# Optimization experiments

Hardware: AMD Instinct MI355X
Metric: run time of the kernel (lower is better)

The kernel has to match this reference:

```python
import jax, jax.numpy as jnp
import numpy as np

D_MODEL = 1024
N_HEADS = 16
TREE_DEPTH = 5
B, T = 2, 1024


def setup_inputs() -> dict:
    key = jax.random.key(0)
    k1, k2, k3, k4 = jax.random.split(key, 4)
    sc = 1.0 / np.sqrt(D_MODEL)
    return {
        "x": jax.random.normal(k1, (B, T, D_MODEL), dtype=jnp.float32),
        "Wp": jax.random.normal(k2, (D_MODEL, N_HEADS * TREE_DEPTH), dtype=jnp.float32) * sc,
        "bp": jnp.zeros((N_HEADS * TREE_DEPTH,), dtype=jnp.float32),
        "Wv": jax.random.normal(k3, (D_MODEL, D_MODEL), dtype=jnp.float32) * sc,
        "Wo": jax.random.normal(k4, (D_MODEL, D_MODEL), dtype=jnp.float32) * sc,
    }


def reference(x, Wp, bp, Wv, Wo):
    Bc, Tc, d = x.shape
    H, Dt = N_HEADS, TREE_DEPTH
    dh = d // H
    # tree paths: (B, H, T, Dt)
    paths = jax.nn.sigmoid(x @ Wp + bp).reshape(Bc, Tc, H, Dt).transpose(0, 2, 1, 3)
    pq = paths[:, :, :, None, :]  # (B,H,T,1,Dt)
    pk = paths[:, :, None, :, :]  # (B,H,1,T,Dt)
    agree = pq * pk + (1.0 - pq) * (1.0 - pk)  # (B,H,T,T,Dt)
    sim = jnp.cumprod(agree, axis=-1).sum(axis=-1) / Dt  # (B,H,T,T)
    # causal mask (strict upper triangle -> -inf)
    causal_mask = jnp.triu(jnp.ones((Tc, Tc), dtype=bool), k=1)
    sim = jnp.where(causal_mask[None, None], -jnp.inf, sim)
    attn = jax.nn.softmax(sim, axis=-1)
    V = (x @ Wv).reshape(Bc, Tc, H, dh).transpose(0, 2, 1, 3)  # (B,H,T,dh)
    ctx = jnp.einsum("bhqk,bhkd->bhqd", attn, V)
    ctx = ctx.transpose(0, 2, 1, 3).reshape(Bc, Tc, d)
    return ctx @ Wo
```

## Files before the change

kernel.cpp:

```cpp
#include <hip/hip_runtime.h>
#include <hip/hip_bf16.h>

#define B_SZ 2
#define T_SEQ 1024
#define D_MODEL 1024
#define N_HEADS 16
#define TREE_DEPTH 5
#define DH 64

typedef __attribute__((ext_vector_type(8))) short short8;
typedef __attribute__((ext_vector_type(4))) float f32x4;

__device__ __forceinline__ ushort f2bf(float f) {
    uint32_t u = __float_as_uint(f);
    u += 0x7FFFu + ((u >> 16) & 1u);
    return (ushort)(u >> 16);
}

__device__ __forceinline__ void gll16(const void* g, void* l) {
    __builtin_amdgcn_global_load_lds(
        (const __attribute__((address_space(1))) void*)g,
        (__attribute__((address_space(3))) void*)l, 16, 0, 0);
}

__global__ __launch_bounds__(256) void prologue(
    const float* __restrict__ x, const float* __restrict__ Wv,
    const float* __restrict__ Wo, const float* __restrict__ Wp,
    ushort* __restrict__ xb, ushort* __restrict__ Wvt,
    ushort* __restrict__ Wot, ushort* __restrict__ Wpt)
{
    __shared__ __align__(16) char sm[20480];
    const int bid = blockIdx.x, tid = threadIdx.x;
    if (bid < 1024) {
        const int i = (bid * 256 + tid) * 8;
        const float4 a = *(const float4*)(x + i);
        const float4 b = *(const float4*)(x + i + 4);
        ushort o[8] = {f2bf(a.x), f2bf(a.y), f2bf(a.z), f2bf(a.w),
                       f2bf(b.x), f2bf(b.y), f2bf(b.z), f2bf(b.w)};
        *(uint4*)(xb + i) = *(const uint4*)o;
    } else if (bid < 3072) {
        const int t = bid - 1024;
        const float* W = (t < 1024) ? Wv : Wo;
        ushort* Wt = (t < 1024) ? Wvt : Wot;
        const int ti = t & 1023;
        const int n0 = (ti & 31) * 32, k0 = (ti >> 5) * 32;
        float (*tile)[33] = (float(*)[33])sm;
        const int tx = tid & 31, ty = tid >> 5;
        #pragma unroll
        for (int i = 0; i < 4; ++i)
            tile[ty + i * 8][tx] = W[(size_t)(k0 + ty + i * 8) * 1024 + n0 + tx];
        __syncthreads();
        #pragma unroll
        for (int i = 0; i < 4; ++i)
            Wt[(size_t)(n0 + ty + i * 8) * 1024 + k0 + tx] = f2bf(tile[tx][ty + i * 8]);
    } else {
        float* tile = (float*)sm;
        const int k0 = (bid - 3072) * 64;
        #pragma unroll
        for (int j = 0; j < 20; ++j) {
            const int i = tid + j * 256;
            tile[i] = Wp[(size_t)k0 * 80 + i];
        }
        __syncthreads();
        #pragma unroll
        for (int j = 0; j < 20; ++j) {
            const int o = tid + j * 256;
            const int n = o >> 6, k = o & 63;
            Wpt[(size_t)n * 1024 + k0 + k] = f2bf(tile[k * 80 + n]);
        }
    }
}

template <bool OUT_BF16>
__device__ __forceinline__ void gemm_body(
    const ushort* __restrict__ A, const ushort* __restrict__ Bt,
    void* __restrict__ Cv, int N, int K, int bx, int by,
    ushort* As, ushort* Bs)
{
    const int tid = threadIdx.x;
    const int lane = tid & 63;
    const int w = tid >> 6;
    const int wm = w & 1, wn = w >> 1;
    const int rowBase = by * 64;
    const int colBase = bx * 64;

    const int srow = lane & 15;
    const int sk = (lane >> 4) * 8;

    const ushort* gA = A + (size_t)(rowBase + w * 16 + srow) * K + sk;
    const ushort* gB = Bt + (size_t)(colBase + w * 16 + srow) * K + sk;

    f32x4 acc[2][2];
    #pragma unroll
    for (int i = 0; i < 2; ++i) {
        acc[i][0] = (f32x4)0.0f;
        acc[i][1] = (f32x4)0.0f;
    }

    gll16(gA,      As + (w * 2 + 0) * 512);
    gll16(gA + 32, As + (w * 2 + 1) * 512);
    gll16(gB,      Bs + (w * 2 + 0) * 512);
    gll16(gB + 32, Bs + (w * 2 + 1) * 512);

    const int niter = K / 64;
    for (int it = 0; it < niter; ++it) {
        __syncthreads();
        const int cur = (it & 1) * 4096;
        if (it + 1 < niter) {
            const int nxt = ((it + 1) & 1) * 4096;
            const int ko = (it + 1) * 64;
            gll16(gA + ko,      As + nxt + (w * 2 + 0) * 512);
            gll16(gA + ko + 32, As + nxt + (w * 2 + 1) * 512);
            gll16(gB + ko,      Bs + nxt + (w * 2 + 0) * 512);
            gll16(gB + ko + 32, Bs + nxt + (w * 2 + 1) * 512);
        }
        #pragma unroll
        for (int ks = 0; ks < 2; ++ks) {
            short8 af[2], bf[2];
            #pragma unroll
            for (int i = 0; i < 2; ++i)
                af[i] = *(const short8*)(As + cur + ((wm * 2 + i) * 2 + ks) * 512 + lane * 8);
            #pragma unroll
            for (int j = 0; j < 2; ++j)
                bf[j] = *(const short8*)(Bs + cur + ((wn * 2 + j) * 2 + ks) * 512 + lane * 8);
            #pragma unroll
            for (int i = 0; i < 2; ++i)
                #pragma unroll
                for (int j = 0; j < 2; ++j)
                    acc[i][j] = __builtin_amdgcn_mfma_f32_16x16x32_bf16(
                        af[i], bf[j], acc[i][j], 0, 0, 0);
        }
    }

    const int quad = lane >> 4, m16 = lane & 15;
    #pragma unroll
    for (int i = 0; i < 2; ++i)
        #pragma unroll
        for (int j = 0; j < 2; ++j) {
            const int col = colBase + wn * 32 + j * 16 + m16;
            #pragma unroll
            for (int r = 0; r < 4; ++r) {
                const int row = rowBase + wm * 32 + i * 16 + quad * 4 + r;
                if (OUT_BF16)
                    ((ushort*)Cv)[(size_t)row * N + col] = f2bf(acc[i][j][r]);
                else
                    ((float*)Cv)[(size_t)row * N + col] = acc[i][j][r];
            }
        }
}

__device__ __forceinline__ void phi_body(
    const ushort* __restrict__ xb, const ushort* __restrict__ Wpt,
    const float* __restrict__ bp, ushort* __restrict__ Phi,
    int blk, float* red, float* p_s)
{
    const int tid = threadIdx.x;
    const int lane = tid & 63, w = tid >> 6;
    const int quad = lane >> 4, m16 = lane & 15;
    const int row0 = blk * 16;

    f32x4 acc[5];
    #pragma unroll
    for (int nb = 0; nb < 5; ++nb) acc[nb] = (f32x4)0.0f;

    const ushort* ap = xb + (size_t)(row0 + m16) * 1024 + w * 256 + quad * 8;
    const ushort* bpz = Wpt + (size_t)m16 * 1024 + w * 256 + quad * 8;
    #pragma unroll
    for (int it = 0; it < 8; ++it) {
        const short8 af = *(const short8*)(ap + it * 32);
        #pragma unroll
        for (int nb = 0; nb < 5; ++nb) {
            const short8 bf = *(const short8*)(bpz + (size_t)nb * 16 * 1024 + it * 32);
            acc[nb] = __builtin_amdgcn_mfma_f32_16x16x32_bf16(af, bf, acc[nb], 0, 0, 0);
        }
    }
    #pragma unroll
    for (int nb = 0; nb < 5; ++nb)
        #pragma unroll
        for (int r = 0; r < 4; ++r)
            red[(w * 16 + quad * 4 + r) * 80 + nb * 16 + m16] = acc[nb][r];
    __syncthreads();
    #pragma unroll
    for (int j = 0; j < 5; ++j) {
        const int i = tid + j * 256;
        const int rr = i / 80, cc = i - rr * 80;
        const float v = red[(0 * 16 + rr) * 80 + cc] + red[(1 * 16 + rr) * 80 + cc] +
                        red[(2 * 16 + rr) * 80 + cc] + red[(3 * 16 + rr) * 80 + cc] + bp[cc];
        p_s[rr * 80 + cc] = 1.0f / (1.0f + __expf(-v));
    }
    __syncthreads();
    #pragma unroll
    for (int j = 0; j < 8; ++j) {
        const int c = tid + j * 256;
        const int rr = c >> 7, rem = c & 127;
        const int h = rem >> 3, f8 = (rem & 7) * 8;
        const float* pr = &p_s[rr * 80 + h * 5];
        ushort o[8];
        #pragma unroll
        for (int e = 0; e < 8; ++e) {
            const int f = f8 + e;
            float val = 0.0f;
            if (f < 62) {
                int d, off;
                if (f < 2)       { d = 1; off = 0; }
                else if (f < 6)  { d = 2; off = 2; }
                else if (f < 14) { d = 3; off = 6; }
                else if (f < 30) { d = 4; off = 14; }
                else             { d = 5; off = 30; }
                const int e2 = f - off;
                float prod = 1.0f;
                for (int jj = 1; jj <= d; ++jj) {
                    const float p = pr[jj - 1];
                    prod *= ((e2 >> (d - jj)) & 1) ? (1.0f - p) : p;
                }
                val = prod;
            }
            o[e] = f2bf(val);
        }
        const int grow = row0 + rr;
        const int b = grow >> 10, t = grow & 1023;
        *(uint4*)(Phi + ((size_t)(b * 16 + h) * 1024 + t) * 64 + f8) =
            *(const uint4*)o;
    }
}

__global__ __launch_bounds__(256) void mid_kernel(
    const ushort* __restrict__ xb, const ushort* __restrict__ Wvt,
    const ushort* __restrict__ Wpt, const float* __restrict__ bp,
    ushort* __restrict__ Vt, ushort* __restrict__ Phi)
{
    __shared__ __align__(16) char sm[32768];
    if (blockIdx.x < 512) {
        ushort* As = (ushort*)sm;
        ushort* Bs = As + 8192;
        gemm_body<true>(Wvt, xb, Vt, 2048, 1024,
                        blockIdx.x & 31, blockIdx.x >> 5, As, Bs);
    } else {
        float* red = (float*)sm;
        float* p_s = (float*)(sm + 20480);
        phi_body(xb, Wpt, bp, Phi, blockIdx.x - 512, red, p_s);
    }
}

__global__ __launch_bounds__(256) void gemm_out(
    const ushort* __restrict__ ctxb, const ushort* __restrict__ Wot,
    float* __restrict__ out)
{
    __shared__ __align__(16) ushort sm[16384];
    gemm_body<false>(ctxb, Wot, out, 1024, 1024,
                     blockIdx.x, blockIdx.y, sm, sm + 8192);
}

__global__ __launch_bounds__(256) void attn_mfma(
    const ushort* __restrict__ Phi, const ushort* __restrict__ Vt,
    ushort* __restrict__ ctxb)
{
    const int qt = 15 - blockIdx.x;
    const int bh = blockIdx.y;
    const int b = bh >> 4, h = bh & 15;
    const int tid = threadIdx.x;
    const int lane = tid & 63;
    const int w = tid >> 6;
    const int quad = lane >> 4, m16 = lane & 15;

    __shared__ __align__(16) ushort K_s[2][4096];
    __shared__ __align__(16) ushort V_s[2][4096];
    __shared__ __align__(16) ushort W_s[4096];
    __shared__ float den_s[4][16];

    const int srow = lane & 15;
    const int sk = (lane >> 4) * 8;
    const ushort* gK = Phi + (size_t)bh * 1024 * 64 + (w * 16 + srow) * 64 + sk;
    const ushort* gV = Vt + (size_t)(h * 64 + w * 16 + srow) * 2048 + b * 1024 + sk;

    const int qglob = qt * 64 + w * 16 + m16;
    const ushort* qbase = Phi + ((size_t)bh * 1024 + qglob) * 64 + quad * 8;
    const short8 qf0 = *(const short8*)qbase;
    const short8 qf1 = *(const short8*)(qbase + 32);

    f32x4 cacc[4];
    #pragma unroll
    for (int nb = 0; nb < 4; ++nb) cacc[nb] = (f32x4)0.0f;
    float den = 0.0f;

    gll16(gK,      K_s[0] + (w * 2 + 0) * 512);
    gll16(gK + 32, K_s[0] + (w * 2 + 1) * 512);
    gll16(gV,      V_s[0] + (w * 2 + 0) * 512);
    gll16(gV + 32, V_s[0] + (w * 2 + 1) * 512);

    const float C = 0.28853901817f;

    for (int kt = 0; kt <= qt; ++kt) {
        const int cur = kt & 1;
        __syncthreads();
        if (kt < qt) {
            const int nxt = cur ^ 1;
            const ushort* nK = gK + (kt + 1) * 4096;
            const ushort* nV = gV + (kt + 1) * 64;
            gll16(nK,      K_s[nxt] + (w * 2 + 0) * 512);
            gll16(nK + 32, K_s[nxt] + (w * 2 + 1) * 512);
            gll16(nV,      V_s[nxt] + (w * 2 + 0) * 512);
            gll16(nV + 32, V_s[nxt] + (w * 2 + 1) * 512);
        }
        const bool diag = (kt == qt);
        #pragma unroll
        for (int nb = 0; nb < 4; ++nb) {
            const short8 kf0 = *(const short8*)(K_s[cur] + (nb * 2 + 0) * 512 + lane * 8);
            const short8 kf1 = *(const short8*)(K_s[cur] + (nb * 2 + 1) * 512 + lane * 8);
            f32x4 s = (f32x4)0.0f;
            s = __builtin_amdgcn_mfma_f32_16x16x32_bf16(kf0, qf0, s, 0, 0, 0);
            s = __builtin_amdgcn_mfma_f32_16x16x32_bf16(kf1, qf1, s, 0, 0, 0);
            ushort o[4];
            if (diag) {
                const int k0g = kt * 64 + nb * 16 + quad * 4;
                #pragma unroll
                for (int r = 0; r < 4; ++r) {
                    float wgt = 0.0f;
                    if (k0g + r <= qglob) wgt = exp2f(s[r] * C);
                    den += wgt;
                    o[r] = f2bf(wgt);
                }
            } else {
                #pragma unroll
                for (int r = 0; r < 4; ++r) {
                    const float wgt = exp2f(s[r] * C);
                    den += wgt;
                    o[r] = f2bf(wgt);
                }
            }
            const int addr = (w * 2 + (nb >> 1)) * 512 +
                             ((nb & 1) * 2 + (quad >> 1)) * 128 +
                             m16 * 8 + (quad & 1) * 4;
            *(uint2*)(W_s + addr) = *(const uint2*)o;
        }
        const short8 wf0 = *(const short8*)(W_s + (w * 2 + 0) * 512 + lane * 8);
        const short8 wf1 = *(const short8*)(W_s + (w * 2 + 1) * 512 + lane * 8);
        #pragma unroll
        for (int nb = 0; nb < 4; ++nb) {
            const short8 vf0 = *(const short8*)(V_s[cur] + (nb * 2 + 0) * 512 + lane * 8);
            const short8 vf1 = *(const short8*)(V_s[cur] + (nb * 2 + 1) * 512 + lane * 8);
            cacc[nb] = __builtin_amdgcn_mfma_f32_16x16x32_bf16(wf0, vf0, cacc[nb], 0, 0, 0);
            cacc[nb] = __builtin_amdgcn_mfma_f32_16x16x32_bf16(wf1, vf1, cacc[nb], 0, 0, 0);
        }
    }

    den += __shfl_xor(den, 16);
    den += __shfl_xor(den, 32);
    den_s[w][m16] = den;
    __syncthreads();
    float inv[4];
    #pragma unroll
    for (int r = 0; r < 4; ++r) inv[r] = 1.0f / den_s[w][quad * 4 + r];

    #pragma unroll
    for (int nb = 0; nb < 4; ++nb) {
        const int dim = h * 64 + nb * 16 + m16;
        #pragma unroll
        for (int r = 0; r < 4; ++r) {
            const int token = qt * 64 + w * 16 + quad * 4 + r;
            ctxb[(size_t)(b * 1024 + token) * D_MODEL + dim] = f2bf(cacc[nb][r] * inv[r]);
        }
    }
}

extern "C" void kernel_launch(void* const* d_in, const int* in_sizes, int n_in,
                              void* d_out, int out_size, void* d_ws, size_t ws_size,
                              hipStream_t stream)
{
    const float* x  = (const float*)d_in[0];
    const float* Wp = (const float*)d_in[1];
    const float* bp = (const float*)d_in[2];
    const float* Wv = (const float*)d_in[3];
    const float* Wo = (const float*)d_in[4];
    float* out = (float*)d_out;

    char* ws = (char*)d_ws;
    ushort* xb   = (ushort*)(ws);
    ushort* Wvt  = (ushort*)(ws + (4u  << 20));
    ushort* Wot  = (ushort*)(ws + (6u  << 20));
    ushort* Phi  = (ushort*)(ws + (8u  << 20));
    ushort* Vt   = (ushort*)(ws + (12u << 20));
    ushort* ctxb = (ushort*)(ws + (16u << 20));
    ushort* Wpt  = (ushort*)(ws + (20u << 20));

    prologue<<<3088, 256, 0, stream>>>(x, Wv, Wo, Wp, xb, Wvt, Wot, Wpt);
    mid_kernel<<<640, 256, 0, stream>>>(xb, Wvt, Wpt, bp, Vt, Phi);
    attn_mfma<<<dim3(16, 32), 256, 0, stream>>>(Phi, Vt, ctxb);
    gemm_out<<<dim3(16, 32), 256, 0, stream>>>(ctxb, Wot, out);
}
```

Before: 151.0 us.

## Load GEMM A operand directly to registers and move Wo transpose into mid kernel

The GEMM body now loads the A operand straight from global memory into registers, prefetching one step ahead, instead of staging it through LDS. Only B stays double-buffered in shared memory, which halves LDS use per block. The Wo transpose/convert work moves from the prologue into mid_kernel so it runs alongside the V GEMM and phi computation, shortening the prologue. The trade-off is more register pressure and uncoalesced-ish per-lane global reads of A, with rows shared between waves now re-fetched by each wave.

Result: slower. 164.2 us (+8.8%).

```diff
diff --git a/kernel.cpp b/kernel.cpp
--- a/kernel.cpp
+++ b/kernel.cpp
@@ -25,9 +25,9 @@
 
 __global__ __launch_bounds__(256) void prologue(
     const float* __restrict__ x, const float* __restrict__ Wv,
-    const float* __restrict__ Wo, const float* __restrict__ Wp,
+    const float* __restrict__ Wp,
     ushort* __restrict__ xb, ushort* __restrict__ Wvt,
-    ushort* __restrict__ Wot, ushort* __restrict__ Wpt)
+    ushort* __restrict__ Wpt)
 {
     __shared__ __align__(16) char sm[20480];
     const int bid = blockIdx.x, tid = threadIdx.x;
@@ -38,24 +38,21 @@
         ushort o[8] = {f2bf(a.x), f2bf(a.y), f2bf(a.z), f2bf(a.w),
                        f2bf(b.x), f2bf(b.y), f2bf(b.z), f2bf(b.w)};
         *(uint4*)(xb + i) = *(const uint4*)o;
-    } else if (bid < 3072) {
-        const int t = bid - 1024;
-        const float* W = (t < 1024) ? Wv : Wo;
-        ushort* Wt = (t < 1024) ? Wvt : Wot;
-        const int ti = t & 1023;
+    } else if (bid < 2048) {
+        const int ti = bid - 1024;
         const int n0 = (ti & 31) * 32, k0 = (ti >> 5) * 32;
         float (*tile)[33] = (float(*)[33])sm;
         const int tx = tid & 31, ty = tid >> 5;
         #pragma unroll
         for (int i = 0; i < 4; ++i)
-            tile[ty + i * 8][tx] = W[(size_t)(k0 + ty + i * 8) * 1024 + n0 + tx];
+            tile[ty + i * 8][tx] = Wv[(size_t)(k0 + ty + i * 8) * 1024 + n0 + tx];
         __syncthreads();
         #pragma unroll
         for (int i = 0; i < 4; ++i)
-            Wt[(size_t)(n0 + ty + i * 8) * 1024 + k0 + tx] = f2bf(tile[tx][ty + i * 8]);
+            Wvt[(size_t)(n0 + ty + i * 8) * 1024 + k0 + tx] = f2bf(tile[tx][ty + i * 8]);
     } else {
         float* tile = (float*)sm;
-        const int k0 = (bid - 3072) * 64;
+        const int k0 = (bid - 2048) * 64;
         #pragma unroll
         for (int j = 0; j < 20; ++j) {
             const int i = tid + j * 256;
@@ -75,7 +72,7 @@
 __device__ __forceinline__ void gemm_body(
     const ushort* __restrict__ A, const ushort* __restrict__ Bt,
     void* __restrict__ Cv, int N, int K, int bx, int by,
-    ushort* As, ushort* Bs)
+    ushort* Bs)
 {
     const int tid = threadIdx.x;
     const int lane = tid & 63;
@@ -87,7 +84,7 @@
     const int srow = lane & 15;
     const int sk = (lane >> 4) * 8;
 
-    const ushort* gA = A + (size_t)(rowBase + w * 16 + srow) * K + sk;
+    const ushort* gA = A + (size_t)(rowBase + wm * 32 + srow) * K + sk;
     const ushort* gB = Bt + (size_t)(colBase + w * 16 + srow) * K + sk;
 
     f32x4 acc[2][2];
@@ -97,29 +94,32 @@
         acc[i][1] = (f32x4)0.0f;
     }
 
-    gll16(gA,      As + (w * 2 + 0) * 512);
-    gll16(gA + 32, As + (w * 2 + 1) * 512);
     gll16(gB,      Bs + (w * 2 + 0) * 512);
     gll16(gB + 32, Bs + (w * 2 + 1) * 512);
+    short8 a[4];
+    a[0] = *(const short8*)(gA);
+    a[1] = *(const short8*)(gA + 32);
+    a[2] = *(const short8*)(gA + (size_t)16 * K);
+    a[3] = *(const short8*)(gA + (size_t)16 * K + 32);
 
     const int niter = K / 64;
     for (int it = 0; it < niter; ++it) {
         __syncthreads();
         const int cur = (it & 1) * 4096;
+        short8 an[4];
         if (it + 1 < niter) {
             const int nxt = ((it + 1) & 1) * 4096;
             const int ko = (it + 1) * 64;
-            gll16(gA + ko,      As + nxt + (w * 2 + 0) * 512);
-            gll16(gA + ko + 32, As + nxt + (w * 2 + 1) * 512);
             gll16(gB + ko,      Bs + nxt + (w * 2 + 0) * 512);
             gll16(gB + ko + 32, Bs + nxt + (w * 2 + 1) * 512);
+            an[0] = *(const short8*)(gA + ko);
+            an[1] = *(const short8*)(gA + ko + 32);
+            an[2] = *(const short8*)(gA + ko + (size_t)16 * K);
+            an[3] = *(const short8*)(gA + ko + (size_t)16 * K + 32);
         }
         #pragma unroll
         for (int ks = 0; ks < 2; ++ks) {
-            short8 af[2], bf[2];
-            #pragma unroll
-            for (int i = 0; i < 2; ++i)
-                af[i] = *(const short8*)(As + cur + ((wm * 2 + i) * 2 + ks) * 512 + lane * 8);
+            short8 bf[2];
             #pragma unroll
             for (int j = 0; j < 2; ++j)
                 bf[j] = *(const short8*)(Bs + cur + ((wn * 2 + j) * 2 + ks) * 512 + lane * 8);
@@ -128,8 +128,10 @@
                 #pragma unroll
                 for (int j = 0; j < 2; ++j)
                     acc[i][j] = __builtin_amdgcn_mfma_f32_16x16x32_bf16(
-                        af[i], bf[j], acc[i][j], 0, 0, 0);
-        }
+                        a[i * 2 + ks], bf[j], acc[i][j], 0, 0, 0);
+        }
+        #pragma unroll
+        for (int i = 0; i < 4; ++i) a[i] = an[i];
     }
 
     const int quad = lane >> 4, m16 = lane & 15;
@@ -227,18 +229,31 @@
 __global__ __launch_bounds__(256) void mid_kernel(
     const ushort* __restrict__ xb, const ushort* __restrict__ Wvt,
     const ushort* __restrict__ Wpt, const float* __restrict__ bp,
-    ushort* __restrict__ Vt, ushort* __restrict__ Phi)
-{
-    __shared__ __align__(16) char sm[32768];
-    if (blockIdx.x < 512) {
-        ushort* As = (ushort*)sm;
-        ushort* Bs = As + 8192;
+    const float* __restrict__ Wo,
+    ushort* __restrict__ Vt, ushort* __restrict__ Phi,
+    ushort* __restrict__ Wot)
+{
+    __shared__ __align__(16) char sm[25600];
+    const int bid = blockIdx.x, tid = threadIdx.x;
+    if (bid < 512) {
         gemm_body<true>(Wvt, xb, Vt, 2048, 1024,
-                        blockIdx.x & 31, blockIdx.x >> 5, As, Bs);
-    } else {
+                        bid & 31, bid >> 5, (ushort*)sm);
+    } else if (bid < 640) {
         float* red = (float*)sm;
         float* p_s = (float*)(sm + 20480);
-        phi_body(xb, Wpt, bp, Phi, blockIdx.x - 512, red, p_s);
+        phi_body(xb, Wpt, bp, Phi, bid - 512, red, p_s);
+    } else {
+        const int ti = bid - 640;
+        const int n0 = (ti & 31) * 32, k0 = (ti >> 5) * 32;
+        float (*tile)[33] = (float(*)[33])sm;
+        const int tx = tid & 31, ty = tid >> 5;
+        #pragma unroll
+        for (int i = 0; i < 4; ++i)
+            tile[ty + i * 8][tx] = Wo[(size_t)(k0 + ty + i * 8) * 1024 + n0 + tx];
+        __syncthreads();
+        #pragma unroll
+        for (int i = 0; i < 4; ++i)
+            Wot[(size_t)(n0 + ty + i * 8) * 1024 + k0 + tx] = f2bf(tile[tx][ty + i * 8]);
     }
 }
 
@@ -246,9 +261,9 @@
     const ushort* __restrict__ ctxb, const ushort* __restrict__ Wot,
     float* __restrict__ out)
 {
-    __shared__ __align__(16) ushort sm[16384];
+    __shared__ __align__(16) ushort sm[8192];
     gemm_body<false>(ctxb, Wot, out, 1024, 1024,
-                     blockIdx.x, blockIdx.y, sm, sm + 8192);
+                     blockIdx.x, blockIdx.y, sm);
 }
 
 __global__ __launch_bounds__(256) void attn_mfma(
@@ -383,8 +398,8 @@
     ushort* ctxb = (ushort*)(ws + (16u << 20));
     ushort* Wpt  = (ushort*)(ws + (20u << 20));
 
-    prologue<<<3088, 256, 0, stream>>>(x, Wv, Wo, Wp, xb, Wvt, Wot, Wpt);
-    mid_kernel<<<640, 256, 0, stream>>>(xb, Wvt, Wpt, bp, Vt, Phi);
+    prologue<<<2064, 256, 0, stream>>>(x, Wv, Wp, xb, Wvt, Wpt);
+    mid_kernel<<<1664, 256, 0, stream>>>(xb, Wvt, Wpt, bp, Wo, Vt, Phi, Wot);
     attn_mfma<<<dim3(16, 32), 256, 0, stream>>>(Phi, Vt, ctxb);
     gemm_out<<<dim3(16, 32), 256, 0, stream>>>(ctxb, Wot, out);
 }
```
